# Kernel optimization log

Hardware: AMD Instinct MI355X
Metric: run time of the kernel (lower is better)

The kernel has to match this reference:

```python
import jax, jax.numpy as jnp
import numpy as np

B, NNODE, E = 262144, 5, 8
NF, EF, D, ED = 7, 2, 16, 4
L = 4  # num_convs
INV = 1.0 / np.sqrt(1.0 + 1e-5)  # BN eval with running_mean=0, running_var=1


def setup_inputs() -> dict:
    key = jax.random.key(0)
    ks = iter(jax.random.split(key, 64))
    r = lambda shape, s=0.1: s * jax.random.normal(next(ks), shape, dtype=jnp.float32)
    g = lambda shape: 1.0 + 0.1 * jax.random.normal(next(ks), shape, dtype=jnp.float32)
    inp = {}
    inp['node_feat'] = jax.random.normal(next(ks), (B, NNODE, NF), dtype=jnp.float32)
    inp['edge_feat'] = jax.random.normal(next(ks), (B, E, EF), dtype=jnp.float32)
    inp['edge_index'] = jax.random.randint(next(ks), (2, E), 0, NNODE)
    # embeddings
    inp['W_ne'] = r((NF, D)); inp['b_ne'] = r((D,))
    inp['g_ne'] = g((NNODE,)); inp['be_ne'] = r((NNODE,))
    inp['W_ee'] = r((EF, ED)); inp['b_ee'] = r((ED,))
    # conv layers (stacked over L)
    inp['msg_W1'] = r((L, 2 * D + ED, D)); inp['msg_b1'] = r((L, D))
    inp['msg_W2'] = r((L, D, D)); inp['msg_b2'] = r((L, D))
    inp['upd_W1'] = r((L, 2 * D, D)); inp['upd_b1'] = r((L, D))
    inp['upd_g1'] = g((L, NNODE)); inp['upd_be1'] = r((L, NNODE))
    inp['upd_W2'] = r((L, D, D)); inp['upd_b2'] = r((L, D))
    inp['upd_g2'] = g((L, NNODE)); inp['upd_be2'] = r((L, NNODE))
    # pool
    inp['Wp'] = r((NNODE * D, D)); inp['bp'] = r((D,))
    inp['gp'] = g((D,)); inp['bep'] = r((D,))
    # MLP head
    inp['mlp_W1'] = r((D, 64)); inp['mlp_b1'] = r((64,)); inp['mlp_g1'] = g((64,)); inp['mlp_be1'] = r((64,))
    inp['mlp_W2'] = r((64, 64)); inp['mlp_b2'] = r((64,)); inp['mlp_g2'] = g((64,)); inp['mlp_be2'] = r((64,))
    inp['mlp_W3'] = r((64, 64)); inp['mlp_b3'] = r((64,)); inp['mlp_g3'] = g((64,)); inp['mlp_be3'] = r((64,))
    inp['mlp_W4'] = r((64, 1)); inp['mlp_b4'] = r((1,))
    return inp


def _bn5(x, gam, bet):  # x: [B,5,D], BatchNorm1d(5) eval over channel dim 1
    return gam[None, :, None] * (x * INV) + bet[None, :, None]


def _bnc(x, gam, bet):  # x: [N,C]
    return gam * (x * INV) + bet


def reference(node_feat, edge_feat, edge_index, W_ne, b_ne, g_ne, be_ne, W_ee, b_ee,
              msg_W1, msg_b1, msg_W2, msg_b2, upd_W1, upd_b1, upd_g1, upd_be1,
              upd_W2, upd_b2, upd_g2, upd_be2, Wp, bp, gp, bep,
              mlp_W1, mlp_b1, mlp_g1, mlp_be1, mlp_W2, mlp_b2, mlp_g2, mlp_be2,
              mlp_W3, mlp_b3, mlp_g3, mlp_be3, mlp_W4, mlp_b4):
    src, dst = edge_index[0], edge_index[1]
    x = _bn5(node_feat @ W_ne + b_ne, g_ne, be_ne)          # [B,5,D]
    ea = edge_feat @ W_ee + b_ee                             # [B,E,ED]
    cnt = jnp.zeros((NNODE,), jnp.float32).at[dst].add(1.0)
    denom = jnp.clip(cnt, 1.0)[None, :, None]
    for l in range(L):
        h_i = x[:, dst, :]                                   # [B,E,D] dest gather
        h_j = x[:, src, :]                                   # [B,E,D] source gather
        m = jnp.concatenate([h_i, h_j, ea], axis=-1)         # [B,E,2D+ED]
        m = jax.nn.sigmoid(m @ msg_W1[l] + msg_b1[l])
        m = jax.nn.sigmoid(m @ msg_W2[l] + msg_b2[l])        # [B,E,D]
        agg = jnp.zeros_like(x).at[:, dst, :].add(m) / denom  # mean scatter -> [B,5,D]
        u = jnp.concatenate([x, agg], axis=-1)               # [B,5,2D]
        u = jax.nn.sigmoid(_bn5(u @ upd_W1[l] + upd_b1[l], upd_g1[l], upd_be1[l]))
        u = jax.nn.sigmoid(_bn5(u @ upd_W2[l] + upd_b2[l], upd_g2[l], upd_be2[l]))
        x = x + u                                            # residual
    p = x.reshape(x.shape[0], NNODE * D)                     # concat of 5 node slots
    p = jax.nn.sigmoid(_bnc(p @ Wp + bp, gp, bep))
    p = jax.nn.sigmoid(_bnc(p @ mlp_W1 + mlp_b1, mlp_g1, mlp_be1))
    p = jax.nn.sigmoid(_bnc(p @ mlp_W2 + mlp_b2, mlp_g2, mlp_be2))
    p = jax.nn.sigmoid(_bnc(p @ mlp_W3 + mlp_b3, mlp_g3, mlp_be3))
    return p @ mlp_W4 + mlp_b4                               # [B,1]
```

## Files before the change

### kernel.cpp

```cpp
#include <hip/hip_runtime.h>

#define NT 256
#define GPB 64
#define NB 262144
#define NCOL 66
#define ROWS 128
#define NSLOT 44
#define INVC 0.9999950000374997f

typedef __attribute__((ext_vector_type(8))) short bf8;
typedef __attribute__((ext_vector_type(4))) float f4;
typedef unsigned int u32;
typedef __attribute__((ext_vector_type(4))) unsigned int u32x4;

struct P {
  const float* node_feat; const float* edge_feat; const int* ei;
  const float* W_ne; const float* b_ne; const float* g_ne; const float* be_ne;
  const float* W_ee; const float* b_ee;
  const float* msg_W1; const float* msg_b1; const float* msg_W2; const float* msg_b2;
  const float* upd_W1; const float* upd_b1; const float* upd_g1; const float* upd_be1;
  const float* upd_W2; const float* upd_b2; const float* upd_g2; const float* upd_be2;
  const float* Wp; const float* bp; const float* gp; const float* bep;
  const float* mW1; const float* mb1; const float* mg1; const float* mbe1;
  const float* mW2; const float* mb2; const float* mg2; const float* mbe2;
  const float* mW3; const float* mb3; const float* mg3; const float* mbe3;
  const float* mW4; const float* mb4;
  float* out; u32* ws;
};

__device__ __forceinline__ float sigm(float x) {
  return __builtin_amdgcn_rcpf(1.0f + __expf(-x));
}

__device__ __forceinline__ u32 pk(float v) {
  u32 u = __builtin_bit_cast(u32, v);
  u32 hi = u & 0xFFFF0000u;
  float res = v - __builtin_bit_cast(float, hi);
  return hi | (__builtin_bit_cast(u32, res) >> 16);
}
__device__ __forceinline__ float upk(u32 p) {
  return __builtin_bit_cast(float, p & 0xFFFF0000u) +
         __builtin_bit_cast(float, p << 16);
}

struct F2 { bf8 h, l; };

__device__ __forceinline__ F2 fragFromU32(const u32 (&x)[8]) {
  u32x4 H, L;
#pragma unroll
  for (int i = 0; i < 4; i++) {
    H[i] = __builtin_amdgcn_perm(x[2 * i + 1], x[2 * i], 0x07060302u);
    L[i] = __builtin_amdgcn_perm(x[2 * i + 1], x[2 * i], 0x05040100u);
  }
  F2 r;
  r.h = __builtin_bit_cast(bf8, H);
  r.l = __builtin_bit_cast(bf8, L);
  return r;
}

__device__ __forceinline__ F2 pack2(const float (&v)[8]) {
  u32 x[8];
#pragma unroll
  for (int i = 0; i < 8; i++) x[i] = pk(v[i]);
  return fragFromU32(x);
}

__device__ __forceinline__ f4 mm(const F2& a, const F2& b, f4 c) {
  c = __builtin_amdgcn_mfma_f32_16x16x32_bf16(a.l, b.h, c, 0, 0, 0);
  c = __builtin_amdgcn_mfma_f32_16x16x32_bf16(a.h, b.l, c, 0, 0, 0);
  c = __builtin_amdgcn_mfma_f32_16x16x32_bf16(a.h, b.h, c, 0, 0, 0);
  return c;
}

__device__ __forceinline__ F2 ldFrag(const u32* ws, int slot, int l) {
  const u32x4* pw = (const u32x4*)(ws + slot * 512 + l * 8);
  F2 r;
  r.h = __builtin_bit_cast(bf8, pw[0]);
  r.l = __builtin_bit_cast(bf8, pw[1]);
  return r;
}

__device__ __forceinline__ F2 packAr(const u32* xb, int row0) {
  u32 x[8];
#pragma unroll
  for (int i = 0; i < 8; i++) x[i] = xb[(row0 + i) * NCOL];
  return fragFromU32(x);
}
__device__ __forceinline__ F2 packA16(const u32* xb, int rowbase, int q) {
  u32 x[8];
#pragma unroll
  for (int i = 0; i < 8; i++) {
    const int k = 8 * (q & 1) + i;
    u32 v = xb[(rowbase + k) * NCOL];
    x[i] = (q < 2) ? v : 0u;
  }
  return fragFromU32(x);
}

__device__ __forceinline__ void wrDp(u32* dst, f4 d) {
  *(uint2*)dst = uint2{pk(d[0]), pk(d[1])};
  *(uint2*)(dst + 2) = uint2{pk(d[2]), pk(d[3])};
}

__device__ __forceinline__ f4 splat4(float b) { return f4{b, b, b, b}; }

__global__ __launch_bounds__(64) void pack_kernel(P pp) {
  const int s = blockIdx.x;
  const int l = threadIdx.x;
  const int q = l >> 4, n = l & 15;
  const float* W; int LD = 16, KV;
  if (s == 0) { W = pp.W_ne; KV = 7; }
  else if (s < 21) {
    const int l4 = (s - 1) / 5, r = (s - 1) % 5;
    if (r == 0)      { W = pp.msg_W1 + l4 * 576;       KV = 32; }
    else if (r == 1) { W = pp.msg_W1 + l4 * 576 + 512; KV = 4;  }
    else if (r == 2) { W = pp.msg_W2 + l4 * 256;       KV = 16; }
    else if (r == 3) { W = pp.upd_W1 + l4 * 512;       KV = 32; }
    else             { W = pp.upd_W2 + l4 * 256;       KV = 16; }
  } else if (s < 24) {
    const int i = s - 21; W = pp.Wp + i * 512; KV = (i < 2) ? 32 : 16;
  } else if (s < 28) {
    W = pp.mW1 + (s - 24) * 16; LD = 64; KV = 16;
  } else if (s < 36) {
    const int i = s - 28; W = pp.mW2 + (i >> 2) * 2048 + (i & 3) * 16; LD = 64; KV = 32;
  } else {
    const int i = s - 36; W = pp.mW3 + (i >> 2) * 2048 + (i & 3) * 16; LD = 64; KV = 32;
  }
  float v[8];
#pragma unroll
  for (int i = 0; i < 8; i++) {
    const int kq = 8 * q + i;
    v[i] = (kq < KV) ? W[kq * LD + n] : 0.f;
  }
  F2 f = pack2(v);
  u32* dst = pp.ws + s * 512 + l * 8;
  *(u32x4*)dst = __builtin_bit_cast(u32x4, f.h);
  *(u32x4*)(dst + 4) = __builtin_bit_cast(u32x4, f.l);
}

__global__ __launch_bounds__(NT, 1) void gnn_kernel(P pp) {
  __shared__ u32 xs32[ROWS][NCOL];

  const int t = threadIdx.x;
  const int w = t >> 6;
  const int l = t & 63;
  const int q = l >> 4;
  const int m16 = l & 15;
  const int col = w * 16 + m16;
  const int cD = w * 16 + 4 * q;
  const int gbase = blockIdx.x * GPB + w * 16;
  const u32* ws = pp.ws;

  const u32* xb = &xs32[0][col];
  const f4 z4 = {0.f, 0.f, 0.f, 0.f};

  int se_[8], de_[8];
#pragma unroll
  for (int e = 0; e < 8; e++) {
    se_[e] = __builtin_amdgcn_readfirstlane(pp.ei[e]);
    de_[e] = __builtin_amdgcn_readfirstlane(pp.ei[8 + e]);
  }
  float dr_[5];
#pragma unroll
  for (int n = 0; n < 5; n++) {
    int c = 0;
#pragma unroll
    for (int e = 0; e < 8; e++) c += (de_[e] == n) ? 1 : 0;
    dr_[n] = 1.0f / (float)(c > 1 ? c : 1);
  }

  {
    F2 Bne = ldFrag(ws, 0, l);
#pragma unroll 1
    for (int n = 0; n < 5; n++) {
      float v[8];
#pragma unroll
      for (int i = 0; i < 8; i++) {
        const int k = 8 * q + i;
        v[i] = (k < 7) ? pp.node_feat[(size_t)(gbase + m16) * 35 + n * 7 + k] : 0.f;
      }
      F2 a = pack2(v);
      f4 d = mm(a, Bne, z4);
      const float gn = pp.g_ne[n] * INVC, bn = pp.be_ne[n];
      f4 o;
#pragma unroll
      for (int r = 0; r < 4; r++) o[r] = fmaf(gn, d[r], bn);
      wrDp(&xs32[n * 16 + m16][cD], o);
    }
  }

  {
#pragma unroll
    for (int s2 = 0; s2 < 2; s2++) {
      const int e = 2 * q + s2;
      const float e0 = pp.edge_feat[(size_t)(gbase + m16) * 16 + 2 * e];
      const float e1 = pp.edge_feat[(size_t)(gbase + m16) * 16 + 2 * e + 1];
#pragma unroll
      for (int j = 0; j < 4; j++) {
        const float val = fmaf(e0, pp.W_ee[j], fmaf(e1, pp.W_ee[4 + j], pp.b_ee[j]));
        xs32[96 + e * 4 + j][col] = pk(val);
      }
    }
  }

#pragma unroll 1
  for (int l4 = 0; l4 < 4; l4++) {
    const int sb = 1 + l4 * 5;
    F2 B1a = ldFrag(ws, sb + 0, l);
    F2 B1e = ldFrag(ws, sb + 1, l);
    F2 B2  = ldFrag(ws, sb + 2, l);
    F2 BU1 = ldFrag(ws, sb + 3, l);
    F2 BU2 = ldFrag(ws, sb + 4, l);
    const float mb1n = pp.msg_b1[l4 * 16 + m16];
    const float mb2n = pp.msg_b2[l4 * 16 + m16];
    const float ub1n = pp.upd_b1[l4 * 16 + m16];
    const float ub2n = pp.upd_b2[l4 * 16 + m16];

    f4 agg[5];
#pragma unroll
    for (int n = 0; n < 5; n++) agg[n] = z4;

#pragma unroll 1
    for (int e = 0; e < 8; e++) {
      const int se = se_[e], de = de_[e];

      u32 xv[8];
#pragma unroll
      for (int j = 0; j < 4; j++) {
        const u32 r = xs32[96 + e * 4 + j][col];
        xv[j] = (q == 0) ? r : 0u;
      }
#pragma unroll
      for (int j = 4; j < 8; j++) xv[j] = 0u;
      F2 aea = fragFromU32(xv);

      f4 c1 = splat4(mb1n);
      c1 = mm(aea, B1e, c1);
      const int rowH = (q < 2) ? de * 16 + 8 * q : se * 16 + 8 * (q - 2);
      F2 ah = packAr(xb, rowH);
      c1 = mm(ah, B1a, c1);
#pragma unroll
      for (int r = 0; r < 4; r++) c1[r] = sigm(c1[r]);
      wrDp(&xs32[80 + m16][cD], c1);
      F2 am = packA16(xb, 80, q);

      f4 c2 = splat4(mb2n);
      c2 = mm(am, B2, c2);
#pragma unroll
      for (int r = 0; r < 4; r++) {
        const float vv = sigm(c2[r]);
        agg[0][r] += (de == 0) ? vv : 0.f;
        agg[1][r] += (de == 1) ? vv : 0.f;
        agg[2][r] += (de == 2) ? vv : 0.f;
        agg[3][r] += (de == 3) ? vv : 0.f;
        agg[4][r] += (de == 4) ? vv : 0.f;
      }
    }

#pragma unroll
    for (int nn = 0; nn < 5; nn++) {
      const float dr = dr_[nn];
      f4 av;
#pragma unroll
      for (int r = 0; r < 4; r++) av[r] = agg[nn][r] * dr;
      wrDp(&xs32[80 + m16][cD], av);
      const int rowU = (q < 2) ? nn * 16 + 8 * q : 80 + 8 * (q - 2);
      F2 au = packAr(xb, rowU);
      f4 c = splat4(ub1n);
      c = mm(au, BU1, c);
      const float G1 = pp.upd_g1[l4 * 5 + nn] * INVC;
      const float Bb1 = pp.upd_be1[l4 * 5 + nn];
#pragma unroll
      for (int r = 0; r < 4; r++) c[r] = sigm(fmaf(G1, c[r], Bb1));
      wrDp(&xs32[80 + m16][cD], c);
      F2 a2 = packA16(xb, 80, q);
      f4 c2 = splat4(ub2n);
      c2 = mm(a2, BU2, c2);
      const float G2 = pp.upd_g2[l4 * 5 + nn] * INVC;
      const float Bb2 = pp.upd_be2[l4 * 5 + nn];
      u32* xp = &xs32[nn * 16 + m16][cD];
      uint2 a01 = *(uint2*)xp;
      uint2 a23 = *(uint2*)(xp + 2);
      a01.x = pk(upk(a01.x) + sigm(fmaf(G2, c2[0], Bb2)));
      a01.y = pk(upk(a01.y) + sigm(fmaf(G2, c2[1], Bb2)));
      a23.x = pk(upk(a23.x) + sigm(fmaf(G2, c2[2], Bb2)));
      a23.y = pk(upk(a23.y) + sigm(fmaf(G2, c2[3], Bb2)));
      *(uint2*)xp = a01;
      *(uint2*)(xp + 2) = a23;
    }
  }

  {
    f4 c = splat4(pp.bp[m16]);
    F2 a0 = packAr(xb, 8 * q);
    c = mm(a0, ldFrag(ws, 21, l), c);
    F2 a1 = packAr(xb, 32 + 8 * q);
    c = mm(a1, ldFrag(ws, 22, l), c);
    F2 a2 = packA16(xb, 64, q);
    c = mm(a2, ldFrag(ws, 23, l), c);
    const float gpn = pp.gp[m16] * INVC, bepn = pp.bep[m16];
    f4 o;
#pragma unroll
    for (int r = 0; r < 4; r++) o[r] = sigm(fmaf(gpn, c[r], bepn));
    wrDp(&xs32[80 + m16][cD], o);
  }

  {
    F2 a = packA16(xb, 80, q);
#pragma unroll 1
    for (int nt = 0; nt < 4; nt++) {
      const int nb = nt * 16 + m16;
      f4 c = splat4(pp.mb1[nb]);
      c = mm(a, ldFrag(ws, 24 + nt, l), c);
      const float g = pp.mg1[nb] * INVC, be = pp.mbe1[nb];
      f4 o;
#pragma unroll
      for (int r = 0; r < 4; r++) o[r] = sigm(fmaf(g, c[r], be));
      wrDp(&xs32[nt * 16 + m16][cD], o);
    }
  }
  {
    F2 a0 = packAr(xb, 8 * q);
    F2 a1 = packAr(xb, 32 + 8 * q);
#pragma unroll 1
    for (int nt = 0; nt < 4; nt++) {
      const int nb = nt * 16 + m16;
      f4 c = splat4(pp.mb2[nb]);
      c = mm(a0, ldFrag(ws, 28 + nt, l), c);
      c = mm(a1, ldFrag(ws, 32 + nt, l), c);
      const float g = pp.mg2[nb] * INVC, be = pp.mbe2[nb];
      f4 o;
#pragma unroll
      for (int r = 0; r < 4; r++) o[r] = sigm(fmaf(g, c[r], be));
      wrDp(&xs32[64 + nt * 16 + m16][cD], o);
    }
  }
  {
    F2 a0 = packAr(xb, 64 + 8 * q);
    F2 a1 = packAr(xb, 96 + 8 * q);
#pragma unroll 1
    for (int nt = 0; nt < 4; nt++) {
      const int nb = nt * 16 + m16;
      f4 c = splat4(pp.mb3[nb]);
      c = mm(a0, ldFrag(ws, 36 + nt, l), c);
      c = mm(a1, ldFrag(ws, 40 + nt, l), c);
      const float g = pp.mg3[nb] * INVC, be = pp.mbe3[nb];
      f4 o;
#pragma unroll
      for (int r = 0; r < 4; r++) o[r] = sigm(fmaf(g, c[r], be));
      wrDp(&xs32[nt * 16 + m16][cD], o);
    }
  }
  {
    float s = 0.f;
#pragma unroll
    for (int j = 0; j < 16; j++)
      s = fmaf(upk(xs32[q * 16 + j][col]), pp.mW4[q * 16 + j], s);
    s += __shfl_down(s, 32);
    s += __shfl_down(s, 16);
    if (l < 16) pp.out[gbase + m16] = s + pp.mb4[0];
  }
}

extern "C" void kernel_launch(void* const* d_in, const int* in_sizes, int n_in,
                              void* d_out, int out_size, void* d_ws, size_t ws_size,
                              hipStream_t stream) {
  P p;
  p.node_feat = (const float*)d_in[0];
  p.edge_feat = (const float*)d_in[1];
  p.ei        = (const int*)d_in[2];
  p.W_ne  = (const float*)d_in[3];  p.b_ne  = (const float*)d_in[4];
  p.g_ne  = (const float*)d_in[5];  p.be_ne = (const float*)d_in[6];
  p.W_ee  = (const float*)d_in[7];  p.b_ee  = (const float*)d_in[8];
  p.msg_W1 = (const float*)d_in[9];  p.msg_b1 = (const float*)d_in[10];
  p.msg_W2 = (const float*)d_in[11]; p.msg_b2 = (const float*)d_in[12];
  p.upd_W1 = (const float*)d_in[13]; p.upd_b1 = (const float*)d_in[14];
  p.upd_g1 = (const float*)d_in[15]; p.upd_be1 = (const float*)d_in[16];
  p.upd_W2 = (const float*)d_in[17]; p.upd_b2 = (const float*)d_in[18];
  p.upd_g2 = (const float*)d_in[19]; p.upd_be2 = (const float*)d_in[20];
  p.Wp  = (const float*)d_in[21]; p.bp  = (const float*)d_in[22];
  p.gp  = (const float*)d_in[23]; p.bep = (const float*)d_in[24];
  p.mW1 = (const float*)d_in[25]; p.mb1 = (const float*)d_in[26];
  p.mg1 = (const float*)d_in[27]; p.mbe1 = (const float*)d_in[28];
  p.mW2 = (const float*)d_in[29]; p.mb2 = (const float*)d_in[30];
  p.mg2 = (const float*)d_in[31]; p.mbe2 = (const float*)d_in[32];
  p.mW3 = (const float*)d_in[33]; p.mb3 = (const float*)d_in[34];
  p.mg3 = (const float*)d_in[35]; p.mbe3 = (const float*)d_in[36];
  p.mW4 = (const float*)d_in[37]; p.mb4 = (const float*)d_in[38];
  p.out = (float*)d_out;
  p.ws  = (u32*)d_ws;

  hipLaunchKernelGGL(pack_kernel, dim3(NSLOT), dim3(64), 0, stream, p);
  hipLaunchKernelGGL(gnn_kernel, dim3(NB / GPB), dim3(NT), 0, stream, p);
}
```

Measured before the change: 285.1 us.

## Fold sigmoid exp scaling into weights, keep residual in registers

```diff
diff --git a/kernel.cpp b/kernel.cpp
--- a/kernel.cpp
+++ b/kernel.cpp
@@ -7,6 +7,7 @@
 #define ROWS 128
 #define NSLOT 44
 #define INVC 0.9999950000374997f
+#define SCL -1.442695040888963f
 
 typedef __attribute__((ext_vector_type(8))) short bf8;
 typedef __attribute__((ext_vector_type(4))) float f4;
@@ -28,8 +29,8 @@
   float* out; u32* ws;
 };
 
-__device__ __forceinline__ float sigm(float x) {
-  return __builtin_amdgcn_rcpf(1.0f + __expf(-x));
+__device__ __forceinline__ float sigm2(float y) {
+  return __builtin_amdgcn_rcpf(1.0f + __builtin_amdgcn_exp2f(y));
 }
 
 __device__ __forceinline__ u32 pk(float v) {
@@ -109,12 +110,15 @@
   const int l = threadIdx.x;
   const int q = l >> 4, n = l & 15;
   const float* W; int LD = 16, KV;
+  const float* brow = nullptr;
+  float scl = 1.0f;
   if (s == 0) { W = pp.W_ne; KV = 7; }
   else if (s < 21) {
     const int l4 = (s - 1) / 5, r = (s - 1) % 5;
-    if (r == 0)      { W = pp.msg_W1 + l4 * 576;       KV = 32; }
-    else if (r == 1) { W = pp.msg_W1 + l4 * 576 + 512; KV = 4;  }
-    else if (r == 2) { W = pp.msg_W2 + l4 * 256;       KV = 16; }
+    if (r == 0)      { W = pp.msg_W1 + l4 * 576;       KV = 32; scl = SCL; }
+    else if (r == 1) { W = pp.msg_W1 + l4 * 576 + 512; KV = 4;  scl = SCL;
+                       brow = pp.msg_b1 + l4 * 16; }
+    else if (r == 2) { W = pp.msg_W2 + l4 * 256;       KV = 16; scl = SCL; }
     else if (r == 3) { W = pp.upd_W1 + l4 * 512;       KV = 32; }
     else             { W = pp.upd_W2 + l4 * 256;       KV = 16; }
   } else if (s < 24) {
@@ -130,7 +134,10 @@
 #pragma unroll
   for (int i = 0; i < 8; i++) {
     const int kq = 8 * q + i;
-    v[i] = (kq < KV) ? W[kq * LD + n] : 0.f;
+    float x = 0.f;
+    if (kq < KV) x = W[kq * LD + n];
+    else if (brow && kq == KV) x = brow[n];
+    v[i] = x * scl;
   }
   F2 f = pack2(v);
   u32* dst = pp.ws + s * 512 + l * 8;
@@ -169,6 +176,7 @@
     dr_[n] = 1.0f / (float)(c > 1 ? c : 1);
   }
 
+  f4 xr[5];
   {
     F2 Bne = ldFrag(ws, 0, l);
 #pragma unroll 1
@@ -182,10 +190,9 @@
       F2 a = pack2(v);
       f4 d = mm(a, Bne, z4);
       const float gn = pp.g_ne[n] * INVC, bn = pp.be_ne[n];
-      f4 o;
-#pragma unroll
-      for (int r = 0; r < 4; r++) o[r] = fmaf(gn, d[r], bn);
-      wrDp(&xs32[n * 16 + m16][cD], o);
+#pragma unroll
+      for (int r = 0; r < 4; r++) xr[n][r] = fmaf(gn, d[r], bn);
+      wrDp(&xs32[n * 16 + m16][cD], xr[n]);
     }
   }
 
@@ -211,8 +218,7 @@
     F2 B2  = ldFrag(ws, sb + 2, l);
     F2 BU1 = ldFrag(ws, sb + 3, l);
     F2 BU2 = ldFrag(ws, sb + 4, l);
-    const float mb1n = pp.msg_b1[l4 * 16 + m16];
-    const float mb2n = pp.msg_b2[l4 * 16 + m16];
+    const float mb2n = pp.msg_b2[l4 * 16 + m16] * SCL;
     const float ub1n = pp.upd_b1[l4 * 16 + m16];
     const float ub2n = pp.upd_b2[l4 * 16 + m16];
 
@@ -230,17 +236,16 @@
         const u32 r = xs32[96 + e * 4 + j][col];
         xv[j] = (q == 0) ? r : 0u;
       }
-#pragma unroll
-      for (int j = 4; j < 8; j++) xv[j] = 0u;
+      xv[4] = (q == 0) ? 0x3F800000u : 0u;
+      xv[5] = xv[6] = xv[7] = 0u;
       F2 aea = fragFromU32(xv);
 
-      f4 c1 = splat4(mb1n);
-      c1 = mm(aea, B1e, c1);
+      f4 c1 = mm(aea, B1e, z4);
       const int rowH = (q < 2) ? de * 16 + 8 * q : se * 16 + 8 * (q - 2);
       F2 ah = packAr(xb, rowH);
       c1 = mm(ah, B1a, c1);
 #pragma unroll
-      for (int r = 0; r < 4; r++) c1[r] = sigm(c1[r]);
+      for (int r = 0; r < 4; r++) c1[r] = sigm2(c1[r]);
       wrDp(&xs32[80 + m16][cD], c1);
       F2 am = packA16(xb, 80, q);
 
@@ -248,7 +253,7 @@
       c2 = mm(am, B2, c2);
 #pragma unroll
       for (int r = 0; r < 4; r++) {
-        const float vv = sigm(c2[r]);
+        const float vv = sigm2(c2[r]);
         agg[0][r] += (de == 0) ? vv : 0.f;
         agg[1][r] += (de == 1) ? vv : 0.f;
         agg[2][r] += (de == 2) ? vv : 0.f;
@@ -268,25 +273,19 @@
       F2 au = packAr(xb, rowU);
       f4 c = splat4(ub1n);
       c = mm(au, BU1, c);
-      const float G1 = pp.upd_g1[l4 * 5 + nn] * INVC;
-      const float Bb1 = pp.upd_be1[l4 * 5 + nn];
-#pragma unroll
-      for (int r = 0; r < 4; r++) c[r] = sigm(fmaf(G1, c[r], Bb1));
+      const float G1 = pp.upd_g1[l4 * 5 + nn] * (SCL * INVC);
+      const float Bb1 = pp.upd_be1[l4 * 5 + nn] * SCL;
+#pragma unroll
+      for (int r = 0; r < 4; r++) c[r] = sigm2(fmaf(G1, c[r], Bb1));
       wrDp(&xs32[80 + m16][cD], c);
       F2 a2 = packA16(xb, 80, q);
       f4 c2 = splat4(ub2n);
       c2 = mm(a2, BU2, c2);
-      const float G2 = pp.upd_g2[l4 * 5 + nn] * INVC;
-      const float Bb2 = pp.upd_be2[l4 * 5 + nn];
-      u32* xp = &xs32[nn * 16 + m16][cD];
-      uint2 a01 = *(uint2*)xp;
-      uint2 a23 = *(uint2*)(xp + 2);
-      a01.x = pk(upk(a01.x) + sigm(fmaf(G2, c2[0], Bb2)));
-      a01.y = pk(upk(a01.y) + sigm(fmaf(G2, c2[1], Bb2)));
-      a23.x = pk(upk(a23.x) + sigm(fmaf(G2, c2[2], Bb2)));
-      a23.y = pk(upk(a23.y) + sigm(fmaf(G2, c2[3], Bb2)));
-      *(uint2*)xp = a01;
-      *(uint2*)(xp + 2) = a23;
+      const float G2 = pp.upd_g2[l4 * 5 + nn] * (SCL * INVC);
+      const float Bb2 = pp.upd_be2[l4 * 5 + nn] * SCL;
+#pragma unroll
+      for (int r = 0; r < 4; r++) xr[nn][r] += sigm2(fmaf(G2, c2[r], Bb2));
+      wrDp(&xs32[nn * 16 + m16][cD], xr[nn]);
     }
   }
 
@@ -298,10 +297,11 @@
     c = mm(a1, ldFrag(ws, 22, l), c);
     F2 a2 = packA16(xb, 64, q);
     c = mm(a2, ldFrag(ws, 23, l), c);
-    const float gpn = pp.gp[m16] * INVC, bepn = pp.bep[m16];
+    const float gpn = pp.gp[m16] * (SCL * INVC);
+    const float bepn = pp.bep[m16] * SCL;
     f4 o;
 #pragma unroll
-    for (int r = 0; r < 4; r++) o[r] = sigm(fmaf(gpn, c[r], bepn));
+    for (int r = 0; r < 4; r++) o[r] = sigm2(fmaf(gpn, c[r], bepn));
     wrDp(&xs32[80 + m16][cD], o);
   }
 
@@ -312,10 +312,10 @@
       const int nb = nt * 16 + m16;
       f4 c = splat4(pp.mb1[nb]);
       c = mm(a, ldFrag(ws, 24 + nt, l), c);
-      const float g = pp.mg1[nb] * INVC, be = pp.mbe1[nb];
+      const float g = pp.mg1[nb] * (SCL * INVC), be = pp.mbe1[nb] * SCL;
       f4 o;
 #pragma unroll
-      for (int r = 0; r < 4; r++) o[r] = sigm(fmaf(g, c[r], be));
+      for (int r = 0; r < 4; r++) o[r] = sigm2(fmaf(g, c[r], be));
       wrDp(&xs32[nt * 16 + m16][cD], o);
     }
   }
@@ -328,10 +328,10 @@
       f4 c = splat4(pp.mb2[nb]);
       c = mm(a0, ldFrag(ws, 28 + nt, l), c);
       c = mm(a1, ldFrag(ws, 32 + nt, l), c);
-      const float g = pp.mg2[nb] * INVC, be = pp.mbe2[nb];
+      const float g = pp.mg2[nb] * (SCL * INVC), be = pp.mbe2[nb] * SCL;
       f4 o;
 #pragma unroll
-      for (int r = 0; r < 4; r++) o[r] = sigm(fmaf(g, c[r], be));
+      for (int r = 0; r < 4; r++) o[r] = sigm2(fmaf(g, c[r], be));
       wrDp(&xs32[64 + nt * 16 + m16][cD], o);
     }
   }
@@ -344,10 +344,10 @@
       f4 c = splat4(pp.mb3[nb]);
       c = mm(a0, ldFrag(ws, 36 + nt, l), c);
       c = mm(a1, ldFrag(ws, 40 + nt, l), c);
-      const float g = pp.mg3[nb] * INVC, be = pp.mbe3[nb];
+      const float g = pp.mg3[nb] * (SCL * INVC), be = pp.mbe3[nb] * SCL;
       f4 o;
 #pragma unroll
-      for (int r = 0; r < 4; r++) o[r] = sigm(fmaf(g, c[r], be));
+      for (int r = 0; r < 4; r++) o[r] = sigm2(fmaf(g, c[r], be));
       wrDp(&xs32[nt * 16 + m16][cD], o);
     }
   }
```

Measured after the change: 279.9 us (median of 2 runs). No clear change (-1.8%).
